# Performance work log

Hardware: AMD Instinct MI355X
Metric: run time of the kernel (lower is better)

The kernel has to match this reference:

```python
import jax, jax.numpy as jnp
import numpy as np

N_NODES = 8   # module-layer pairs
N_EDGES = 32  # connections, 4 outgoing per node
B, H, W = 4, 1024, 1024
EXC_RATIO, EXC_VAL, INH_VAL = 0.8, 1.0, -0.5


def setup_inputs() -> dict:
    key = jax.random.key(0)
    k_sp, k_m, k_w = jax.random.split(key, 3)
    # binary spikes per source node: [N, B, H, W]
    spikes = (jax.random.uniform(k_sp, (N_NODES, B, H, W)) < 0.1).astype(jnp.float32)
    # excitatory/inhibitory mask per source node: [N, H, W]
    u = jax.random.uniform(k_m, (N_NODES, H, W))
    masks = jnp.where(u < EXC_RATIO, EXC_VAL, INH_VAL).astype(jnp.float32)
    # per-connection weight (randn * strength): [E, H, W]
    weights = jax.random.normal(k_w, (N_EDGES, H, W), dtype=jnp.float32) * 0.5
    # edge list: node i -> (i+1..i+4) mod N
    src_idx = jnp.repeat(jnp.arange(N_NODES), 4)
    dst_idx = (src_idx + jnp.tile(jnp.arange(1, 5), N_NODES)) % N_NODES
    return {"spikes": spikes, "masks": masks, "weights": weights,
            "src_idx": src_idx, "dst_idx": dst_idx}


def reference(spikes, masks, weights, src_idx, dst_idx):
    # per-edge signal: gather src spikes, modulate by src mask and edge weight
    # [E, B, H, W] = [E, B, H, W] * [E, 1, H, W] * [E, 1, H, W]
    sig = spikes[src_idx] * masks[src_idx][:, None] * weights[:, None]
    # scatter-sum into destination nodes: [N, B, H, W]
    out = jax.ops.segment_sum(sig, dst_idx, num_segments=spikes.shape[0])
    return out
```

## Files before the change

### kernel.cpp

```cpp
#include <hip/hip_runtime.h>


#define HW (1024 * 1024)
#define NN 8
#define NB 4

__global__ __launch_bounds__(256) void axon_kernel(
    const float* __restrict__ spikes,
    const float* __restrict__ masks,
    const float* __restrict__ weights,
    float* __restrict__ out)
{
    const int t = blockIdx.x * blockDim.x + threadIdx.x;
    const int p = t * 2;

    float2 m[NN];
#pragma unroll
    for (int n = 0; n < NN; ++n)
        m[n] = *reinterpret_cast<const float2*>(masks + n * HW + p);

    float2 mw[32];
#pragma unroll
    for (int e = 0; e < 32; ++e) {
        const float2 w = *reinterpret_cast<const float2*>(weights + e * HW + p);
        mw[e].x = m[e >> 2].x * w.x;
        mw[e].y = m[e >> 2].y * w.y;
    }

#pragma unroll
    for (int b = 0; b < NB; ++b) {
        float2 s[NN];
#pragma unroll
        for (int n = 0; n < NN; ++n)
            s[n] = *reinterpret_cast<const float2*>(spikes + (n * NB + b) * HW + p);

        float2 acc[NN];
#pragma unroll
        for (int n = 0; n < NN; ++n) { acc[n].x = 0.0f; acc[n].y = 0.0f; }

#pragma unroll
        for (int e = 0; e < 32; ++e) {
            const int src = e >> 2;
            const int dst = (src + (e & 3) + 1) & 7;
            acc[dst].x = fmaf(s[src].x, mw[e].x, acc[dst].x);
            acc[dst].y = fmaf(s[src].y, mw[e].y, acc[dst].y);
        }

#pragma unroll
        for (int n = 0; n < NN; ++n)
            *reinterpret_cast<float2*>(out + (n * NB + b) * HW + p) = acc[n];
    }
}

extern "C" void kernel_launch(void* const* d_in, const int* in_sizes, int n_in,
                              void* d_out, int out_size, void* d_ws, size_t ws_size,
                              hipStream_t stream) {
    const float* spikes  = (const float*)d_in[0];
    const float* masks   = (const float*)d_in[1];
    const float* weights = (const float*)d_in[2];
    float* out = (float*)d_out;

    const int threads = 256;
    const int blocks  = (HW / 2) / threads;
    axon_kernel<<<blocks, threads, 0, stream>>>(spikes, masks, weights, out);
}
```

Baseline: 104.4 us.

## Reorder loops by source node, fold mask into spikes, stream stores nontemporally

The loop order is inverted so each source node's mask, spikes and four edge weights are loaded together. The mask is folded into the spikes and results accumulate into a per-destination, per-batch register array that is written once at the end. Edge weights are no longer held in 32 registers across all batches, and outputs use nontemporal stores, aiming to cut cache pollution. Launch bounds now request 4 blocks per SM, which may constrain registers given the 32-element accumulator array.

After: 92.37 us. -11.6%, faster.

```diff
diff --git a/kernel.cpp b/kernel.cpp
--- a/kernel.cpp
+++ b/kernel.cpp
@@ -5,7 +5,9 @@
 #define NN 8
 #define NB 4
 
-__global__ __launch_bounds__(256) void axon_kernel(
+typedef float f32x2 __attribute__((ext_vector_type(2)));
+
+__global__ __launch_bounds__(256, 4) void axon_kernel(
     const float* __restrict__ spikes,
     const float* __restrict__ masks,
     const float* __restrict__ weights,
@@ -14,42 +16,43 @@
     const int t = blockIdx.x * blockDim.x + threadIdx.x;
     const int p = t * 2;
 
-    float2 m[NN];
+    f32x2 acc[NN][NB];
 #pragma unroll
     for (int n = 0; n < NN; ++n)
-        m[n] = *reinterpret_cast<const float2*>(masks + n * HW + p);
+#pragma unroll
+        for (int b = 0; b < NB; ++b) acc[n][b] = (f32x2)(0.0f);
 
-    float2 mw[32];
 #pragma unroll
-    for (int e = 0; e < 32; ++e) {
-        const float2 w = *reinterpret_cast<const float2*>(weights + e * HW + p);
-        mw[e].x = m[e >> 2].x * w.x;
-        mw[e].y = m[e >> 2].y * w.y;
+    for (int src = 0; src < NN; ++src) {
+        const f32x2 m = *reinterpret_cast<const f32x2*>(masks + src * HW + p);
+
+        f32x2 s[NB];
+#pragma unroll
+        for (int b = 0; b < NB; ++b)
+            s[b] = *reinterpret_cast<const f32x2*>(spikes + (src * NB + b) * HW + p);
+
+#pragma unroll
+        for (int b = 0; b < NB; ++b) s[b] *= m;
+
+#pragma unroll
+        for (int k = 0; k < 4; ++k) {
+            const int e   = src * 4 + k;
+            const int dst = (src + k + 1) & 7;
+            const f32x2 w = *reinterpret_cast<const f32x2*>(weights + e * HW + p);
+#pragma unroll
+            for (int b = 0; b < NB; ++b) {
+                acc[dst][b].x = fmaf(s[b].x, w.x, acc[dst][b].x);
+                acc[dst][b].y = fmaf(s[b].y, w.y, acc[dst][b].y);
+            }
+        }
     }
 
 #pragma unroll
-    for (int b = 0; b < NB; ++b) {
-        float2 s[NN];
+    for (int n = 0; n < NN; ++n)
 #pragma unroll
-        for (int n = 0; n < NN; ++n)
-            s[n] = *reinterpret_cast<const float2*>(spikes + (n * NB + b) * HW + p);
-
-        float2 acc[NN];
-#pragma unroll
-        for (int n = 0; n < NN; ++n) { acc[n].x = 0.0f; acc[n].y = 0.0f; }
-
-#pragma unroll
-        for (int e = 0; e < 32; ++e) {
-            const int src = e >> 2;
-            const int dst = (src + (e & 3) + 1) & 7;
-            acc[dst].x = fmaf(s[src].x, mw[e].x, acc[dst].x);
-            acc[dst].y = fmaf(s[src].y, mw[e].y, acc[dst].y);
-        }
-
-#pragma unroll
-        for (int n = 0; n < NN; ++n)
-            *reinterpret_cast<float2*>(out + (n * NB + b) * HW + p) = acc[n];
-    }
+        for (int b = 0; b < NB; ++b)
+            __builtin_nontemporal_store(
+                acc[n][b], reinterpret_cast<f32x2*>(out + (n * NB + b) * HW + p));
 }
 
 extern "C" void kernel_launch(void* const* d_in, const int* in_sizes, int n_in,
```
